# Kernel optimization log

Hardware: AMD Instinct MI355X
Metric: run time of the kernel (lower is better)

Reference implementation:

```python
import jax, jax.numpy as jnp
import numpy as np

ALPHA = 0.01  # LeakyReLU negative slope


def setup_inputs() -> dict:
    key = jax.random.key(0)
    k1, k2, k3 = jax.random.split(key, 3)
    B, T, F, U, E = 32, 512, 128, 64, 32
    x = jax.random.normal(k1, (B, T, F), dtype=jnp.float32)
    Wg = jax.random.normal(k2, (F, E), dtype=jnp.float32) * (1.0 / np.sqrt(F))
    bg = jnp.zeros((E,), dtype=jnp.float32)
    We = jax.random.normal(k3, (E, F, U), dtype=jnp.float32) * (1.0 / np.sqrt(F))
    be = jnp.zeros((E, U), dtype=jnp.float32)
    return {"x": x, "Wg": Wg, "bg": bg, "We": We, "be": be}


def reference(x, Wg, bg, We, be):
    # gate: linear (no softmax in the original)
    gate = jnp.einsum('btf,fe->bte', x, Wg) + bg            # [B,T,E]
    # all experts as one batched GEMM: [B,T,U,E]
    h = jnp.einsum('btf,efu->btue', x, We) + be.T            # be.T: [U,E]
    h = jnp.where(h >= 0, h, ALPHA * h)                      # LeakyReLU
    # weighted sum over experts
    out = jnp.einsum('btue,bte->btu', h, gate)               # [B,T,U]
    return out
```

## Files before the change

### kernel.cpp

```cpp
#include <hip/hip_runtime.h>
#include <stdint.h>

#define N_TOK 16384
#define F_DIM 128
#define U_DIM 64
#define E_DIM 32

typedef __bf16 bf16x8 __attribute__((ext_vector_type(8)));
typedef float  floatx4 __attribute__((ext_vector_type(4)));

#define MFMA16(a, b, c) __builtin_amdgcn_mfma_f32_16x16x32_bf16((a), (b), (c), 0, 0, 0)

__device__ __forceinline__ unsigned short f2bf(float f) {
  union { float f; unsigned u; } v; v.f = f;
  unsigned r = v.u + 0x7FFFu + ((v.u >> 16) & 1u);
  return (unsigned short)(r >> 16);
}

__global__ __launch_bounds__(256) void moe_prep(
    const float* __restrict__ Wg, const float* __restrict__ We,
    unsigned short* __restrict__ wsWe, unsigned short* __restrict__ wsWg) {
  int t = blockIdx.x * 256 + threadIdx.x;
  if (t < 32768) {
    int u = t & 63, quad = (t >> 6) & 3, ks = (t >> 8) & 3, e = t >> 10;
    int f0 = ks * 32 + quad * 8;
    const float* src = We + e * 8192 + f0 * 64 + u;
    union { unsigned short us[8]; uint4 q; } p;
#pragma unroll
    for (int j = 0; j < 8; j++) p.us[j] = f2bf(src[j * 64]);
    *(uint4*)(wsWe + t * 8) = p.q;
  } else if (t < 32768 + 512) {
    int t2 = t - 32768;
    int l15 = t2 & 15, quad = (t2 >> 4) & 3, ks = (t2 >> 6) & 3, et = t2 >> 8;
    int e = et * 16 + l15, f0 = ks * 32 + quad * 8;
    union { unsigned short us[8]; uint4 q; } p;
#pragma unroll
    for (int j = 0; j < 8; j++) p.us[j] = f2bf(Wg[(f0 + j) * 32 + e]);
    *(uint4*)(wsWg + t2 * 8) = p.q;
  }
}

__global__ __launch_bounds__(512, 2) void moe_main(
    const float* __restrict__ x,
    const float* __restrict__ bg,
    const float* __restrict__ be,
    const unsigned short* __restrict__ wsWe,
    const unsigned short* __restrict__ wsWg,
    float* __restrict__ out) {
  __shared__ unsigned short Xs[64 * 136];
  __shared__ float Gs[E_DIM][68];

  const int tid  = threadIdx.x;
  const int lane = tid & 63;
  const int wid  = tid >> 6;
  const int quad = lane >> 4;
  const int l15  = lane & 15;
  const int wr   = wid >> 2;
  const int wc   = wid & 3;
  const int u    = wc * 16 + l15;
  const int base = blockIdx.x * 64;

  bf16x8 bbuf[4][4];
  float bevb[4];
#pragma unroll
  for (int e0 = 0; e0 < 3; e0++) {
#pragma unroll
    for (int ks = 0; ks < 4; ks++)
      bbuf[e0][ks] = *(const bf16x8*)(wsWe + (size_t)((e0 * 4 + ks) * 4 + quad) * 512 + u * 8);
    bevb[e0] = be[e0 * U_DIM + u];
  }

  {
    const int row = tid >> 3;
    const int c16 = tid & 7;
    const float4* src = (const float4*)(x + (size_t)(base + row) * F_DIM + c16 * 16);
    float4 v0 = src[0], v1 = src[1], v2 = src[2], v3 = src[3];
    union { unsigned short us[16]; uint4 q[2]; } pk;
    pk.us[0]  = f2bf(v0.x); pk.us[1]  = f2bf(v0.y); pk.us[2]  = f2bf(v0.z); pk.us[3]  = f2bf(v0.w);
    pk.us[4]  = f2bf(v1.x); pk.us[5]  = f2bf(v1.y); pk.us[6]  = f2bf(v1.z); pk.us[7]  = f2bf(v1.w);
    pk.us[8]  = f2bf(v2.x); pk.us[9]  = f2bf(v2.y); pk.us[10] = f2bf(v2.z); pk.us[11] = f2bf(v2.w);
    pk.us[12] = f2bf(v3.x); pk.us[13] = f2bf(v3.y); pk.us[14] = f2bf(v3.z); pk.us[15] = f2bf(v3.w);
    uint4* dst = (uint4*)&Xs[row * 136 + c16 * 16];
    dst[0] = pk.q[0];
    dst[1] = pk.q[1];
  }
  __syncthreads();

  {
    const int rg = wid >> 1;
    const int et = wid & 1;
    bf16x8 ag[4];
#pragma unroll
    for (int ks = 0; ks < 4; ks++)
      ag[ks] = *(const bf16x8*)&Xs[(rg * 16 + l15) * 136 + ks * 32 + quad * 8];
    floatx4 g = {0.f, 0.f, 0.f, 0.f};
#pragma unroll
    for (int ks = 0; ks < 4; ks++) {
      bf16x8 wb = *(const bf16x8*)(wsWg + (size_t)((et * 4 + ks) * 64 + lane) * 8);
      g = MFMA16(ag[ks], wb, g);
    }
    float bgv = bg[et * 16 + l15];
#pragma unroll
    for (int r = 0; r < 4; r++)
      Gs[et * 16 + l15][rg * 16 + quad * 4 + r] = g[r] + bgv;
  }

  bf16x8 a[2][4];
#pragma unroll
  for (int mb = 0; mb < 2; mb++)
#pragma unroll
    for (int ks = 0; ks < 4; ks++)
      a[mb][ks] = *(const bf16x8*)&Xs[(wr * 32 + mb * 16 + l15) * 136 + ks * 32 + quad * 8];
  __syncthreads();

  float oacc[8];
#pragma unroll
  for (int i = 0; i < 8; i++) oacc[i] = 0.f;

  float4 gbuf[2][2];
#pragma unroll
  for (int mb = 0; mb < 2; mb++)
    gbuf[0][mb] = *(const float4*)&Gs[0][wr * 32 + mb * 16 + quad * 4];

#pragma unroll 4
  for (int e = 0; e < E_DIM; ++e) {
    const int c = e & 3;
    const int gp = e & 1;

    if (e + 3 < E_DIM) {
#pragma unroll
      for (int ks = 0; ks < 4; ks++)
        bbuf[(e + 3) & 3][ks] =
            *(const bf16x8*)(wsWe + (size_t)(((e + 3) * 4 + ks) * 4 + quad) * 512 + u * 8);
      bevb[(e + 3) & 3] = be[(e + 3) * U_DIM + u];
    }
    if (e + 1 < E_DIM) {
#pragma unroll
      for (int mb = 0; mb < 2; mb++)
        gbuf[gp ^ 1][mb] = *(const float4*)&Gs[e + 1][wr * 32 + mb * 16 + quad * 4];
    }

    const float bev = bevb[c];
    floatx4 h[2];
#pragma unroll
    for (int mb = 0; mb < 2; mb++) h[mb] = {bev, bev, bev, bev};
#pragma unroll
    for (int ks = 0; ks < 4; ks++)
#pragma unroll
      for (int mb = 0; mb < 2; mb++)
        h[mb] = MFMA16(a[mb][ks], bbuf[c][ks], h[mb]);

#pragma unroll
    for (int mb = 0; mb < 2; mb++) {
      const float4 g4 = gbuf[gp][mb];
      const float gr[4] = {g4.x, g4.y, g4.z, g4.w};
#pragma unroll
      for (int r = 0; r < 4; r++) {
        float t = h[mb][r];
        t = fmaxf(t, 0.01f * t);
        oacc[mb * 4 + r] = fmaf(gr[r], t, oacc[mb * 4 + r]);
      }
    }
  }

#pragma unroll
  for (int mb = 0; mb < 2; mb++)
#pragma unroll
    for (int r = 0; r < 4; r++)
      out[(size_t)(base + wr * 32 + mb * 16 + quad * 4 + r) * U_DIM + u] = oacc[mb * 4 + r];
}

extern "C" void kernel_launch(void* const* d_in, const int* in_sizes, int n_in,
                              void* d_out, int out_size, void* d_ws, size_t ws_size,
                              hipStream_t stream) {
  const float* x  = (const float*)d_in[0];
  const float* Wg = (const float*)d_in[1];
  const float* bg = (const float*)d_in[2];
  const float* We = (const float*)d_in[3];
  const float* be = (const float*)d_in[4];
  unsigned short* wsWe = (unsigned short*)d_ws;
  unsigned short* wsWg = wsWe + E_DIM * U_DIM * F_DIM;
  (void)in_sizes; (void)n_in; (void)out_size; (void)ws_size;

  moe_prep<<<130, 256, 0, stream>>>(Wg, We, wsWe, wsWg);
  moe_main<<<N_TOK / 64, 512, 0, stream>>>(x, bg, be, wsWe, wsWg, (float*)d_out);
}
```

Measured before the change: 79.74 us.

## Fuse weight conversion into main kernel with double-buffered LDS expert staging

Removes the separate prep kernel that converted We and Wg to bf16 in a workspace. Each block now loads fp32 expert weights directly, converts them to bf16, and stages them through a double-buffered shared-memory tile, with a barrier after every expert. This saves one launch and the workspace round trip. In exchange, all 256 blocks redo the full weight conversion, global fp32 weight traffic per block doubles, LDS use grows by 32KB, and 31 extra barriers are added.

```diff
diff --git a/kernel.cpp b/kernel.cpp
--- a/kernel.cpp
+++ b/kernel.cpp
@@ -17,38 +17,30 @@
   return (unsigned short)(r >> 16);
 }
 
-__global__ __launch_bounds__(256) void moe_prep(
-    const float* __restrict__ Wg, const float* __restrict__ We,
-    unsigned short* __restrict__ wsWe, unsigned short* __restrict__ wsWg) {
-  int t = blockIdx.x * 256 + threadIdx.x;
-  if (t < 32768) {
-    int u = t & 63, quad = (t >> 6) & 3, ks = (t >> 8) & 3, e = t >> 10;
-    int f0 = ks * 32 + quad * 8;
-    const float* src = We + e * 8192 + f0 * 64 + u;
-    union { unsigned short us[8]; uint4 q; } p;
-#pragma unroll
-    for (int j = 0; j < 8; j++) p.us[j] = f2bf(src[j * 64]);
-    *(uint4*)(wsWe + t * 8) = p.q;
-  } else if (t < 32768 + 512) {
-    int t2 = t - 32768;
-    int l15 = t2 & 15, quad = (t2 >> 4) & 3, ks = (t2 >> 6) & 3, et = t2 >> 8;
-    int e = et * 16 + l15, f0 = ks * 32 + quad * 8;
-    union { unsigned short us[8]; uint4 q; } p;
-#pragma unroll
-    for (int j = 0; j < 8; j++) p.us[j] = f2bf(Wg[(f0 + j) * 32 + e]);
-    *(uint4*)(wsWg + t2 * 8) = p.q;
-  }
-}
-
-__global__ __launch_bounds__(512, 2) void moe_main(
+__device__ __forceinline__ uint4 pack8(const float* w) {
+  union { unsigned short us[8]; uint4 q; } p;
+#pragma unroll
+  for (int j = 0; j < 8; j++) p.us[j] = f2bf(w[j]);
+  return p.q;
+}
+
+__device__ __forceinline__ bf16x8 cvt8(const float* w) {
+  union { unsigned short us[8]; bf16x8 v; } p;
+#pragma unroll
+  for (int j = 0; j < 8; j++) p.us[j] = f2bf(w[j]);
+  return p.v;
+}
+
+__global__ __launch_bounds__(512, 2) void moe_fused(
     const float* __restrict__ x,
+    const float* __restrict__ Wg,
     const float* __restrict__ bg,
+    const float* __restrict__ We,
     const float* __restrict__ be,
-    const unsigned short* __restrict__ wsWe,
-    const unsigned short* __restrict__ wsWg,
     float* __restrict__ out) {
-  __shared__ unsigned short Xs[64 * 136];
-  __shared__ float Gs[E_DIM][68];
+  __shared__ __align__(16) unsigned short Xs[64 * 136];
+  __shared__ __align__(16) float Gs[E_DIM][68];
+  __shared__ __align__(16) unsigned short Bs[2][8192];
 
   const int tid  = threadIdx.x;
   const int lane = tid & 63;
@@ -60,15 +52,23 @@
   const int u    = wc * 16 + l15;
   const int base = blockIdx.x * 64;
 
-  bf16x8 bbuf[4][4];
-  float bevb[4];
-#pragma unroll
-  for (int e0 = 0; e0 < 3; e0++) {
-#pragma unroll
-    for (int ks = 0; ks < 4; ks++)
-      bbuf[e0][ks] = *(const bf16x8*)(wsWe + (size_t)((e0 * 4 + ks) * 4 + quad) * 512 + u * 8);
-    bevb[e0] = be[e0 * U_DIM + u];
-  }
+  const float* wsrc0 = We + wid * 512 + lane;
+  const float* wsrc1 = We + (wid + 8) * 512 + lane;
+
+  float w0[8], w1[8];
+#pragma unroll
+  for (int j = 0; j < 8; j++) { w0[j] = wsrc0[j * 64]; w1[j] = wsrc1[j * 64]; }
+
+  const int et = wid & 1;
+  const int rg = wid >> 1;
+  float wgv[4][8];
+#pragma unroll
+  for (int ks = 0; ks < 4; ks++)
+#pragma unroll
+    for (int j = 0; j < 8; j++)
+      wgv[ks][j] = Wg[(ks * 32 + quad * 8 + j) * 32 + et * 16 + l15];
+
+  float bev = be[u];
 
   {
     const int row = tid >> 3;
@@ -86,9 +86,15 @@
   }
   __syncthreads();
 
+  *(uint4*)&Bs[0][tid * 8]        = pack8(w0);
+  *(uint4*)&Bs[0][tid * 8 + 4096] = pack8(w1);
+#pragma unroll
+  for (int j = 0; j < 8; j++) {
+    w0[j] = wsrc0[8192 + j * 64];
+    w1[j] = wsrc1[8192 + j * 64];
+  }
+
   {
-    const int rg = wid >> 1;
-    const int et = wid & 1;
     bf16x8 ag[4];
 #pragma unroll
     for (int ks = 0; ks < 4; ks++)
@@ -96,7 +102,7 @@
     floatx4 g = {0.f, 0.f, 0.f, 0.f};
 #pragma unroll
     for (int ks = 0; ks < 4; ks++) {
-      bf16x8 wb = *(const bf16x8*)(wsWg + (size_t)((et * 4 + ks) * 64 + lane) * 8);
+      bf16x8 wb = cvt8(wgv[ks]);
       g = MFMA16(ag[ks], wb, g);
     }
     float bgv = bg[et * 16 + l15];
@@ -122,33 +128,43 @@
   for (int mb = 0; mb < 2; mb++)
     gbuf[0][mb] = *(const float4*)&Gs[0][wr * 32 + mb * 16 + quad * 4];
 
-#pragma unroll 4
+#pragma unroll
   for (int e = 0; e < E_DIM; ++e) {
-    const int c = e & 3;
+    const int p  = e & 1;
     const int gp = e & 1;
 
-    if (e + 3 < E_DIM) {
-#pragma unroll
-      for (int ks = 0; ks < 4; ks++)
-        bbuf[(e + 3) & 3][ks] =
-            *(const bf16x8*)(wsWe + (size_t)(((e + 3) * 4 + ks) * 4 + quad) * 512 + u * 8);
-      bevb[(e + 3) & 3] = be[(e + 3) * U_DIM + u];
-    }
+    bf16x8 bb[4];
+#pragma unroll
+    for (int ks = 0; ks < 4; ks++)
+      bb[ks] = *(const bf16x8*)&Bs[p][(ks * 4 + quad) * 512 + u * 8];
+
+    if (e + 1 < E_DIM) {
+      *(uint4*)&Bs[p ^ 1][tid * 8]        = pack8(w0);
+      *(uint4*)&Bs[p ^ 1][tid * 8 + 4096] = pack8(w1);
+    }
+    if (e + 2 < E_DIM) {
+#pragma unroll
+      for (int j = 0; j < 8; j++) {
+        w0[j] = wsrc0[(e + 2) * 8192 + j * 64];
+        w1[j] = wsrc1[(e + 2) * 8192 + j * 64];
+      }
+    }
+    float bev_nxt = (e + 1 < E_DIM) ? be[(e + 1) * U_DIM + u] : 0.f;
+
     if (e + 1 < E_DIM) {
 #pragma unroll
       for (int mb = 0; mb < 2; mb++)
         gbuf[gp ^ 1][mb] = *(const float4*)&Gs[e + 1][wr * 32 + mb * 16 + quad * 4];
     }
 
-    const float bev = bevb[c];
     floatx4 h[2];
 #pragma unroll
-    for (int mb = 0; mb < 2; mb++) h[mb] = {bev, bev, bev, bev};
+    for (int mb = 0; mb < 2; mb++) h[mb] = {0.f, 0.f, 0.f, 0.f};
 #pragma unroll
     for (int ks = 0; ks < 4; ks++)
 #pragma unroll
       for (int mb = 0; mb < 2; mb++)
-        h[mb] = MFMA16(a[mb][ks], bbuf[c][ks], h[mb]);
+        h[mb] = MFMA16(a[mb][ks], bb[ks], h[mb]);
 
 #pragma unroll
     for (int mb = 0; mb < 2; mb++) {
@@ -156,11 +172,14 @@
       const float gr[4] = {g4.x, g4.y, g4.z, g4.w};
 #pragma unroll
       for (int r = 0; r < 4; r++) {
-        float t = h[mb][r];
+        float t = h[mb][r] + bev;
         t = fmaxf(t, 0.01f * t);
         oacc[mb * 4 + r] = fmaf(gr[r], t, oacc[mb * 4 + r]);
       }
     }
+    bev = bev_nxt;
+
+    if (e + 1 < E_DIM) __syncthreads();
   }
 
 #pragma unroll
@@ -178,10 +197,7 @@
   const float* bg = (const float*)d_in[2];
   const float* We = (const float*)d_in[3];
   const float* be = (const float*)d_in[4];
-  unsigned short* wsWe = (unsigned short*)d_ws;
-  unsigned short* wsWg = wsWe + E_DIM * U_DIM * F_DIM;
-  (void)in_sizes; (void)n_in; (void)out_size; (void)ws_size;
-
-  moe_prep<<<130, 256, 0, stream>>>(Wg, We, wsWe, wsWg);
-  moe_main<<<N_TOK / 64, 512, 0, stream>>>(x, bg, be, wsWe, wsWg, (float*)d_out);
-}
+  (void)in_sizes; (void)n_in; (void)out_size; (void)d_ws; (void)ws_size;
+
+  moe_fused<<<N_TOK / 64, 512, 0, stream>>>(x, Wg, bg, We, be, (float*)d_out);
+}
```

Result: slower. 180.6 us (+126.5%).

## Stage expert weights through LDS with triple-buffered async global-to-LDS loads

Applied to the files above, without the earlier changes.

Replaces per-wave register prefetch of the expert weights from global memory with a block-wide triple-buffered pipeline. It uses global_load_lds to copy each expert's 16KB weight slice into shared memory, with explicit vmcnt waits and barriers. It also swizzles the X tile in LDS to drop padding and bank conflicts, and stages the expert biases into LDS. Each weight slice is now fetched once per block instead of once per wave. The cost is a 64KB LDS footprint, which may cap occupancy at one block per CU, plus a barrier on every expert iteration.

```diff
diff --git a/kernel.cpp b/kernel.cpp
--- a/kernel.cpp
+++ b/kernel.cpp
@@ -15,6 +15,12 @@
   union { float f; unsigned u; } v; v.f = f;
   unsigned r = v.u + 0x7FFFu + ((v.u >> 16) & 1u);
   return (unsigned short)(r >> 16);
+}
+
+__device__ __forceinline__ void gload_lds16(const void* g, void* l) {
+  __builtin_amdgcn_global_load_lds(
+      (const __attribute__((address_space(1))) unsigned int*)g,
+      (__attribute__((address_space(3))) unsigned int*)l, 16, 0, 0);
 }
 
 __global__ __launch_bounds__(256) void moe_prep(
@@ -47,8 +53,13 @@
     const unsigned short* __restrict__ wsWe,
     const unsigned short* __restrict__ wsWg,
     float* __restrict__ out) {
-  __shared__ unsigned short Xs[64 * 136];
-  __shared__ float Gs[E_DIM][68];
+  __shared__ __align__(16) char smem[65536];
+  unsigned short* Xs  = (unsigned short*)smem;
+  unsigned short* Bs0 = (unsigned short*)(smem + 16384);
+  unsigned short* Bs1 = (unsigned short*)(smem + 32768);
+  unsigned short* Bs2 = (unsigned short*)smem;
+  float* Gs  = (float*)(smem + 49152);
+  float* BeS = (float*)(smem + 57344);
 
   const int tid  = threadIdx.x;
   const int lane = tid & 63;
@@ -60,15 +71,14 @@
   const int u    = wc * 16 + l15;
   const int base = blockIdx.x * 64;
 
-  bf16x8 bbuf[4][4];
-  float bevb[4];
-#pragma unroll
-  for (int e0 = 0; e0 < 3; e0++) {
-#pragma unroll
-    for (int ks = 0; ks < 4; ks++)
-      bbuf[e0][ks] = *(const bf16x8*)(wsWe + (size_t)((e0 * 4 + ks) * 4 + quad) * 512 + u * 8);
-    bevb[e0] = be[e0 * U_DIM + u];
-  }
+  const char* gW = (const char*)wsWe;
+
+  gload_lds16(gW + tid * 16,               Bs0 + tid * 8);
+  gload_lds16(gW + 8192 + tid * 16,        Bs0 + tid * 8 + 4096);
+  gload_lds16(gW + 16384 + tid * 16,       Bs1 + tid * 8);
+  gload_lds16(gW + 16384 + 8192 + tid * 16, Bs1 + tid * 8 + 4096);
+
+  ((float4*)BeS)[tid] = ((const float4*)be)[tid];
 
   {
     const int row = tid >> 3;
@@ -80,9 +90,9 @@
     pk.us[4]  = f2bf(v1.x); pk.us[5]  = f2bf(v1.y); pk.us[6]  = f2bf(v1.z); pk.us[7]  = f2bf(v1.w);
     pk.us[8]  = f2bf(v2.x); pk.us[9]  = f2bf(v2.y); pk.us[10] = f2bf(v2.z); pk.us[11] = f2bf(v2.w);
     pk.us[12] = f2bf(v3.x); pk.us[13] = f2bf(v3.y); pk.us[14] = f2bf(v3.z); pk.us[15] = f2bf(v3.w);
-    uint4* dst = (uint4*)&Xs[row * 136 + c16 * 16];
-    dst[0] = pk.q[0];
-    dst[1] = pk.q[1];
+    const int sw = row & 7;
+    *(uint4*)&Xs[row * 128 + ((c16 * 2) ^ sw) * 8]     = pk.q[0];
+    *(uint4*)&Xs[row * 128 + ((c16 * 2 + 1) ^ sw) * 8] = pk.q[1];
   }
   __syncthreads();
 
@@ -91,8 +101,10 @@
     const int et = wid & 1;
     bf16x8 ag[4];
 #pragma unroll
-    for (int ks = 0; ks < 4; ks++)
-      ag[ks] = *(const bf16x8*)&Xs[(rg * 16 + l15) * 136 + ks * 32 + quad * 8];
+    for (int ks = 0; ks < 4; ks++) {
+      const int row = rg * 16 + l15;
+      ag[ks] = *(const bf16x8*)&Xs[row * 128 + (((ks * 4 + quad) ^ (row & 7))) * 8];
+    }
     floatx4 g = {0.f, 0.f, 0.f, 0.f};
 #pragma unroll
     for (int ks = 0; ks < 4; ks++) {
@@ -102,61 +114,131 @@
     float bgv = bg[et * 16 + l15];
 #pragma unroll
     for (int r = 0; r < 4; r++)
-      Gs[et * 16 + l15][rg * 16 + quad * 4 + r] = g[r] + bgv;
+      Gs[(et * 16 + l15) * 64 + rg * 16 + quad * 4 + r] = g[r] + bgv;
   }
 
   bf16x8 a[2][4];
 #pragma unroll
   for (int mb = 0; mb < 2; mb++)
 #pragma unroll
-    for (int ks = 0; ks < 4; ks++)
-      a[mb][ks] = *(const bf16x8*)&Xs[(wr * 32 + mb * 16 + l15) * 136 + ks * 32 + quad * 8];
+    for (int ks = 0; ks < 4; ks++) {
+      const int row = wr * 32 + mb * 16 + l15;
+      a[mb][ks] = *(const bf16x8*)&Xs[row * 128 + (((ks * 4 + quad) ^ (row & 7))) * 8];
+    }
   __syncthreads();
 
   float oacc[8];
 #pragma unroll
   for (int i = 0; i < 8; i++) oacc[i] = 0.f;
 
-  float4 gbuf[2][2];
-#pragma unroll
-  for (int mb = 0; mb < 2; mb++)
-    gbuf[0][mb] = *(const float4*)&Gs[0][wr * 32 + mb * 16 + quad * 4];
-
-#pragma unroll 4
-  for (int e = 0; e < E_DIM; ++e) {
-    const int c = e & 3;
-    const int gp = e & 1;
-
-    if (e + 3 < E_DIM) {
-#pragma unroll
-      for (int ks = 0; ks < 4; ks++)
-        bbuf[(e + 3) & 3][ks] =
-            *(const bf16x8*)(wsWe + (size_t)(((e + 3) * 4 + ks) * 4 + quad) * 512 + u * 8);
-      bevb[(e + 3) & 3] = be[(e + 3) * U_DIM + u];
-    }
-    if (e + 1 < E_DIM) {
+  const unsigned short* pr0 = Bs0;
+  const unsigned short* pr1 = Bs1;
+  const unsigned short* pr2 = Bs2;
+  const char* gsrc = gW + 2 * 16384;
+
+#pragma unroll 3
+  for (int e = 0; e < 30; ++e) {
+    gload_lds16(gsrc + tid * 16,        (void*)(pr2 + tid * 8));
+    gload_lds16(gsrc + 8192 + tid * 16, (void*)(pr2 + tid * 8 + 4096));
+    gsrc += 16384;
+
+    bf16x8 bb[4];
+#pragma unroll
+    for (int ks = 0; ks < 4; ks++)
+      bb[ks] = *(const bf16x8*)(pr0 + (ks * 4 + quad) * 512 + u * 8);
+    float bev = BeS[e * 64 + u];
+    float4 gc[2];
+#pragma unroll
+    for (int mb = 0; mb < 2; mb++)
+      gc[mb] = *(const float4*)&Gs[e * 64 + wr * 32 + mb * 16 + quad * 4];
+
+    asm volatile("s_waitcnt lgkmcnt(0)" ::: "memory");
+    __builtin_amdgcn_sched_barrier(0);
+
+    floatx4 h[2];
+#pragma unroll
+    for (int mb = 0; mb < 2; mb++) h[mb] = {0.f, 0.f, 0.f, 0.f};
+#pragma unroll
+    for (int ks = 0; ks < 4; ks++)
 #pragma unroll
       for (int mb = 0; mb < 2; mb++)
-        gbuf[gp ^ 1][mb] = *(const float4*)&Gs[e + 1][wr * 32 + mb * 16 + quad * 4];
-    }
-
-    const float bev = bevb[c];
+        h[mb] = MFMA16(a[mb][ks], bb[ks], h[mb]);
+
+#pragma unroll
+    for (int mb = 0; mb < 2; mb++) {
+      const float gr[4] = {gc[mb].x, gc[mb].y, gc[mb].z, gc[mb].w};
+#pragma unroll
+      for (int r = 0; r < 4; r++) {
+        float t = h[mb][r] + bev;
+        t = fmaxf(t, 0.01f * t);
+        oacc[mb * 4 + r] = fmaf(gr[r], t, oacc[mb * 4 + r]);
+      }
+    }
+
+    asm volatile("s_waitcnt vmcnt(2)" ::: "memory");
+    __builtin_amdgcn_s_barrier();
+
+    const unsigned short* t0 = pr0; pr0 = pr1; pr1 = pr2; pr2 = t0;
+  }
+
+  {
+    bf16x8 bb[4];
+#pragma unroll
+    for (int ks = 0; ks < 4; ks++)
+      bb[ks] = *(const bf16x8*)(pr0 + (ks * 4 + quad) * 512 + u * 8);
+    float bev = BeS[30 * 64 + u];
+    float4 gc[2];
+#pragma unroll
+    for (int mb = 0; mb < 2; mb++)
+      gc[mb] = *(const float4*)&Gs[30 * 64 + wr * 32 + mb * 16 + quad * 4];
+    asm volatile("s_waitcnt lgkmcnt(0)" ::: "memory");
+    __builtin_amdgcn_sched_barrier(0);
     floatx4 h[2];
 #pragma unroll
-    for (int mb = 0; mb < 2; mb++) h[mb] = {bev, bev, bev, bev};
+    for (int mb = 0; mb < 2; mb++) h[mb] = {0.f, 0.f, 0.f, 0.f};
 #pragma unroll
     for (int ks = 0; ks < 4; ks++)
 #pragma unroll
       for (int mb = 0; mb < 2; mb++)
-        h[mb] = MFMA16(a[mb][ks], bbuf[c][ks], h[mb]);
-
+        h[mb] = MFMA16(a[mb][ks], bb[ks], h[mb]);
 #pragma unroll
     for (int mb = 0; mb < 2; mb++) {
-      const float4 g4 = gbuf[gp][mb];
-      const float gr[4] = {g4.x, g4.y, g4.z, g4.w};
+      const float gr[4] = {gc[mb].x, gc[mb].y, gc[mb].z, gc[mb].w};
 #pragma unroll
       for (int r = 0; r < 4; r++) {
-        float t = h[mb][r];
+        float t = h[mb][r] + bev;
+        t = fmaxf(t, 0.01f * t);
+        oacc[mb * 4 + r] = fmaf(gr[r], t, oacc[mb * 4 + r]);
+      }
+    }
+    asm volatile("s_waitcnt vmcnt(0)" ::: "memory");
+    __builtin_amdgcn_s_barrier();
+  }
+
+  {
+    bf16x8 bb[4];
+#pragma unroll
+    for (int ks = 0; ks < 4; ks++)
+      bb[ks] = *(const bf16x8*)(pr1 + (ks * 4 + quad) * 512 + u * 8);
+    float bev = BeS[31 * 64 + u];
+    float4 gc[2];
+#pragma unroll
+    for (int mb = 0; mb < 2; mb++)
+      gc[mb] = *(const float4*)&Gs[31 * 64 + wr * 32 + mb * 16 + quad * 4];
+    floatx4 h[2];
+#pragma unroll
+    for (int mb = 0; mb < 2; mb++) h[mb] = {0.f, 0.f, 0.f, 0.f};
+#pragma unroll
+    for (int ks = 0; ks < 4; ks++)
+#pragma unroll
+      for (int mb = 0; mb < 2; mb++)
+        h[mb] = MFMA16(a[mb][ks], bb[ks], h[mb]);
+#pragma unroll
+    for (int mb = 0; mb < 2; mb++) {
+      const float gr[4] = {gc[mb].x, gc[mb].y, gc[mb].z, gc[mb].w};
+#pragma unroll
+      for (int r = 0; r < 4; r++) {
+        float t = h[mb][r] + bev;
         t = fmaxf(t, 0.01f * t);
         oacc[mb * 4 + r] = fmaf(gr[r], t, oacc[mb * 4 + r]);
       }
```

Measured after the change: 84.23 us. +5.6%, slower.

## Fuse weight bf16 conversion into main kernel, drop separate prep launch

Applied to the files above, without the earlier changes.

Removes the moe_prep kernel, which packed We and Wg into bf16 MFMA-ready layouts in a workspace. The main kernel now reads fp32 weights directly with strided scalar loads, holds a 4-stage fp32 prefetch buffer in registers, and converts to bf16 each expert iteration. This saves a kernel launch and the workspace round trip. In exchange it issues many more scalar global loads per block, repeats the conversion work in every block, and drops launch bounds occupancy from 2 to 1 blocks per CU because of the larger register footprint.

```diff
diff --git a/kernel.cpp b/kernel.cpp
--- a/kernel.cpp
+++ b/kernel.cpp
@@ -17,35 +17,12 @@
   return (unsigned short)(r >> 16);
 }
 
-__global__ __launch_bounds__(256) void moe_prep(
-    const float* __restrict__ Wg, const float* __restrict__ We,
-    unsigned short* __restrict__ wsWe, unsigned short* __restrict__ wsWg) {
-  int t = blockIdx.x * 256 + threadIdx.x;
-  if (t < 32768) {
-    int u = t & 63, quad = (t >> 6) & 3, ks = (t >> 8) & 3, e = t >> 10;
-    int f0 = ks * 32 + quad * 8;
-    const float* src = We + e * 8192 + f0 * 64 + u;
-    union { unsigned short us[8]; uint4 q; } p;
-#pragma unroll
-    for (int j = 0; j < 8; j++) p.us[j] = f2bf(src[j * 64]);
-    *(uint4*)(wsWe + t * 8) = p.q;
-  } else if (t < 32768 + 512) {
-    int t2 = t - 32768;
-    int l15 = t2 & 15, quad = (t2 >> 4) & 3, ks = (t2 >> 6) & 3, et = t2 >> 8;
-    int e = et * 16 + l15, f0 = ks * 32 + quad * 8;
-    union { unsigned short us[8]; uint4 q; } p;
-#pragma unroll
-    for (int j = 0; j < 8; j++) p.us[j] = f2bf(Wg[(f0 + j) * 32 + e]);
-    *(uint4*)(wsWg + t2 * 8) = p.q;
-  }
-}
-
-__global__ __launch_bounds__(512, 2) void moe_main(
+__global__ __launch_bounds__(512, 1) void moe_main(
     const float* __restrict__ x,
+    const float* __restrict__ Wg,
     const float* __restrict__ bg,
+    const float* __restrict__ We,
     const float* __restrict__ be,
-    const unsigned short* __restrict__ wsWe,
-    const unsigned short* __restrict__ wsWg,
     float* __restrict__ out) {
   __shared__ unsigned short Xs[64 * 136];
   __shared__ float Gs[E_DIM][68];
@@ -60,14 +37,19 @@
   const int u    = wc * 16 + l15;
   const int base = blockIdx.x * 64;
 
-  bf16x8 bbuf[4][4];
+  float bw[4][4][8];
   float bevb[4];
+  {
+    const float* wsrc = We + (size_t)(quad * 8) * 64 + u;
 #pragma unroll
-  for (int e0 = 0; e0 < 3; e0++) {
+    for (int e0 = 0; e0 < 3; e0++) {
 #pragma unroll
-    for (int ks = 0; ks < 4; ks++)
-      bbuf[e0][ks] = *(const bf16x8*)(wsWe + (size_t)((e0 * 4 + ks) * 4 + quad) * 512 + u * 8);
-    bevb[e0] = be[e0 * U_DIM + u];
+      for (int ks = 0; ks < 4; ks++)
+#pragma unroll
+        for (int j = 0; j < 8; j++)
+          bw[e0][ks][j] = wsrc[(size_t)e0 * 8192 + (ks * 32 + j) * 64];
+      bevb[e0] = be[e0 * U_DIM + u];
+    }
   }
 
   {
@@ -96,8 +78,11 @@
     floatx4 g = {0.f, 0.f, 0.f, 0.f};
 #pragma unroll
     for (int ks = 0; ks < 4; ks++) {
-      bf16x8 wb = *(const bf16x8*)(wsWg + (size_t)((et * 4 + ks) * 64 + lane) * 8);
-      g = MFMA16(ag[ks], wb, g);
+      union { unsigned short us[8]; bf16x8 v; } p;
+#pragma unroll
+      for (int j = 0; j < 8; j++)
+        p.us[j] = f2bf(Wg[(size_t)(ks * 32 + quad * 8 + j) * 32 + et * 16 + l15]);
+      g = MFMA16(ag[ks], p.v, g);
     }
     float bgv = bg[et * 16 + l15];
 #pragma unroll
@@ -122,6 +107,8 @@
   for (int mb = 0; mb < 2; mb++)
     gbuf[0][mb] = *(const float4*)&Gs[0][wr * 32 + mb * 16 + quad * 4];
 
+  const float* wbase = We + (size_t)(quad * 8) * 64 + u;
+
 #pragma unroll 4
   for (int e = 0; e < E_DIM; ++e) {
     const int c = e & 3;
@@ -130,14 +117,24 @@
     if (e + 3 < E_DIM) {
 #pragma unroll
       for (int ks = 0; ks < 4; ks++)
-        bbuf[(e + 3) & 3][ks] =
-            *(const bf16x8*)(wsWe + (size_t)(((e + 3) * 4 + ks) * 4 + quad) * 512 + u * 8);
+#pragma unroll
+        for (int j = 0; j < 8; j++)
+          bw[(e + 3) & 3][ks][j] = wbase[(size_t)(e + 3) * 8192 + (ks * 32 + j) * 64];
       bevb[(e + 3) & 3] = be[(e + 3) * U_DIM + u];
     }
     if (e + 1 < E_DIM) {
 #pragma unroll
       for (int mb = 0; mb < 2; mb++)
         gbuf[gp ^ 1][mb] = *(const float4*)&Gs[e + 1][wr * 32 + mb * 16 + quad * 4];
+    }
+
+    bf16x8 bb[4];
+#pragma unroll
+    for (int ks = 0; ks < 4; ks++) {
+      union { unsigned short us[8]; bf16x8 v; } p;
+#pragma unroll
+      for (int j = 0; j < 8; j++) p.us[j] = f2bf(bw[c][ks][j]);
+      bb[ks] = p.v;
     }
 
     const float bev = bevb[c];
@@ -148,7 +145,7 @@
     for (int ks = 0; ks < 4; ks++)
 #pragma unroll
       for (int mb = 0; mb < 2; mb++)
-        h[mb] = MFMA16(a[mb][ks], bbuf[c][ks], h[mb]);
+        h[mb] = MFMA16(a[mb][ks], bb[ks], h[mb]);
 
 #pragma unroll
     for (int mb = 0; mb < 2; mb++) {
@@ -178,10 +175,7 @@
   const float* bg = (const float*)d_in[2];
   const float* We = (const float*)d_in[3];
   const float* be = (const float*)d_in[4];
-  unsigned short* wsWe = (unsigned short*)d_ws;
-  unsigned short* wsWg = wsWe + E_DIM * U_DIM * F_DIM;
-  (void)in_sizes; (void)n_in; (void)out_size; (void)ws_size;
+  (void)in_sizes; (void)n_in; (void)out_size; (void)d_ws; (void)ws_size;
 
-  moe_prep<<<130, 256, 0, stream>>>(Wg, We, wsWe, wsWg);
-  moe_main<<<N_TOK / 64, 512, 0, stream>>>(x, bg, be, wsWe, wsWg, (float*)d_out);
+  moe_main<<<N_TOK / 64, 512, 0, stream>>>(x, Wg, bg, We, be, (float*)d_out);
 }
```

Result: slower. 97.54 us (+22.3%).
